# Kernel tuning notes

Measured on AMD Instinct MI355X. Metric: run time of the kernel, lower is better.

## Reference

```python
import jax, jax.numpy as jnp
import numpy as np

E = 1024      # emb_size == hidden_size
H = 8         # n_heads
BATCH = 8
NUM = 48      # table rows
KW = 48       # table columns (keys)
L = NUM * KW  # 2304


def _mha(q_in, kv_in, length, Wq, bq, Wk, bk, Wv, bv, Wo, bo, n_heads=H):
    # q_in: (B, T, E), kv_in: (B, S, E); returns (T, B, E) per the torch layout.
    B, T, Em = q_in.shape
    S = kv_in.shape[1]
    dh = Em // n_heads
    q = (q_in @ Wq + bq).reshape(B, T, n_heads, dh).transpose(0, 2, 1, 3)
    k = (kv_in @ Wk + bk).reshape(B, S, n_heads, dh).transpose(0, 2, 1, 3)
    v = (kv_in @ Wv + bv).reshape(B, S, n_heads, dh).transpose(0, 2, 1, 3)
    scores = jnp.einsum('bhtd,bhsd->bhts', q, k) / jnp.asarray(np.sqrt(dh), q.dtype)
    mask = jnp.arange(S) < length  # memory_lengths masking
    scores = jnp.where(mask[None, None, None, :], scores, jnp.finfo(scores.dtype).min)
    attn = jax.nn.softmax(scores, axis=-1)
    out = jnp.einsum('bhts,bhsd->bhtd', attn, v).transpose(0, 2, 1, 3).reshape(B, T, Em)
    out = out @ Wo + bo
    return out.transpose(1, 0, 2)  # (T, B, E)


def setup_inputs() -> dict:
    key = jax.random.key(0)
    ks = jax.random.split(key, 24)

    def W(k, shape, s=0.03):
        return jax.random.normal(k, shape, dtype=jnp.float32) * s

    inp = {
        'emb': jax.random.normal(ks[0], (L, BATCH, E), dtype=jnp.float32),
        # col attention params
        'Wq_c': W(ks[1], (E, E)), 'bq_c': jnp.zeros((E,), jnp.float32),
        'Wk_c': W(ks[2], (E, E)), 'bk_c': jnp.zeros((E,), jnp.float32),
        'Wv_c': W(ks[3], (E, E)), 'bv_c': jnp.zeros((E,), jnp.float32),
        'Wo_c': W(ks[4], (E, E)), 'bo_c': jnp.zeros((E,), jnp.float32),
        # row attention params
        'Wq_r': W(ks[5], (E, E)), 'bq_r': jnp.zeros((E,), jnp.float32),
        'Wk_r': W(ks[6], (E, E)), 'bk_r': jnp.zeros((E,), jnp.float32),
        'Wv_r': W(ks[7], (E, E)), 'bv_r': jnp.zeros((E,), jnp.float32),
        'Wo_r': W(ks[8], (E, E)), 'bo_r': jnp.zeros((E,), jnp.float32),
        # fusion layers
        'W_gen': W(ks[9], (2 * E, E)),
        'W_mlp1': W(ks[10], (2 * E, E)),
        'W_mlp2': W(ks[11], (E, 1)),
        # scalar forward args
        'start_id': 0, 'end_id': L - 1,
        'num': NUM, 'num_tensor': NUM,
        'kw_num': KW, 'kw_num_tensor': KW,
        'batch': BATCH,
    }
    return inp


def reference(emb, Wq_c, bq_c, Wk_c, bk_c, Wv_c, bv_c, Wo_c, bo_c,
              Wq_r, bq_r, Wk_r, bk_r, Wv_r, bv_r, Wo_r, bo_r,
              W_gen, W_mlp1, W_mlp2,
              start_id, end_id, num, num_tensor, kw_num, kw_num_tensor, batch):
    Em = emb.shape[-1]
    length = end_id - start_id + 1  # = num * kw_num
    # emb.narrow(0, start_id, length): (L, batch, E)
    rep = emb[start_id:start_id + length]
    # -> (kw_num, batch*num, E)
    home_ply_rep = rep.transpose(1, 0, 2).reshape(batch * num, kw_num, Em).transpose(1, 0, 2)

    # --- column-dim encoding: attention over the `num` (row) axis ---
    col_mb = jnp.swapaxes(home_ply_rep.reshape(kw_num, batch, num, Em), 0, 2)  # (num, batch, kw, E)
    col_mb = col_mb.reshape(num, batch * kw_num, Em)
    col_q = col_mb.transpose(1, 0, 2)  # (batch*kw, num, E)
    col_rep = _mha(col_q, col_q, num_tensor, Wq_c, bq_c, Wk_c, bk_c, Wv_c, bv_c, Wo_c, bo_c)
    # (num, batch*kw, E) -> (kw_num, batch*num, E)
    col_dim_rep = jnp.swapaxes(col_rep.reshape(num, batch, kw_num, Em), 0, 2).reshape(kw_num, batch * num, Em)

    # --- row-dim encoding: attention over the `kw_num` (column) axis ---
    row_q = col_dim_rep.transpose(1, 0, 2)  # (batch*num, kw, E)
    row_dim_rep = _mha(row_q, row_q, kw_num_tensor, Wq_r, bq_r, Wk_r, bk_r, Wv_r, bv_r, Wo_r, bo_r)  # (kw, b*n, E)

    # --- fusion: concat + Linear + tanh, MLP scores, softmax over {row, col} ---
    gen_rep = jnp.tanh(jnp.concatenate([row_dim_rep, col_dim_rep], axis=-1) @ W_gen)

    def mlp_score(x):
        return jnp.tanh(jnp.concatenate([x, gen_rep], axis=-1) @ W_mlp1) @ W_mlp2  # (kw, b*n, 1)

    row_score = mlp_score(row_dim_rep)
    col_score = mlp_score(col_dim_rep)
    w = jax.nn.softmax(jnp.concatenate([row_score, col_score], axis=-1), axis=-1)  # (kw, b*n, 2)
    home_ply_memory_bank = w[..., 0:1] * row_dim_rep + w[..., 1:2] * col_dim_rep
    # no_fusion=True -> residual add
    home_ply_memory_bank = home_ply_memory_bank + home_ply_rep

    row_for_ptr = row_dim_rep.reshape(kw_num, batch, num, Em)
    col_for_ptr = col_dim_rep.reshape(kw_num, batch, num, Em)

    # row_aggregation == 'mean'
    home_ply_row_rep = home_ply_memory_bank.mean(axis=0)  # (batch*num, E)
    home_ply_row_rep = home_ply_row_rep.reshape(batch, num, Em).transpose(1, 0, 2)  # (num, batch, E)
    return (home_ply_row_rep, home_ply_memory_bank, col_for_ptr, row_for_ptr)
```

## Files before the change

### kernel.cpp

```cpp
#include <hip/hip_runtime.h>
#include <hip/hip_bf16.h>
#include <stdint.h>

typedef unsigned short u16;
typedef unsigned int   u32;
typedef __attribute__((ext_vector_type(4))) float f32x4;
typedef __attribute__((ext_vector_type(2))) float f32x2;
typedef __attribute__((ext_vector_type(8))) short s16x8;

#define DEV __device__ __forceinline__

static constexpr int EDIM  = 1024;
static constexpr int MROWS = 8 * 48 * 48;

DEV float b2f(u16 x) { u32 u = ((u32)x) << 16; float f; __builtin_memcpy(&f, &u, 4); return f; }
DEV u16 f2b(float f) {
    u32 u; __builtin_memcpy(&u, &f, 4);
    u32 r = (u + 0x7FFFu + ((u >> 16) & 1u)) >> 16;
    return (u16)r;
}

#define GLDS16(gsrc, ldst) __builtin_amdgcn_global_load_lds( \
    (const __attribute__((address_space(1))) u32*)(gsrc),    \
    (__attribute__((address_space(3))) u32*)(ldst), 16, 0, 0)

#define BAR()   __builtin_amdgcn_s_barrier()
#define LGKM0() asm volatile("s_waitcnt lgkmcnt(0)" ::: "memory")

enum { F_WRC = 1, F_PERM = 2, F_TANH = 4, F_SCORE = 8, F_OMAP1 = 16, F_OMAP2 = 32 };

struct GJob {
    const u16* A1; const u16* A2; const u16* Bt; const float* bias;
    u16* C; float* outF; const float* w2; float* score;
    int lda, lda2, ldc, KTOT, M, flags, tileEnd, pad;
};
struct GSet { int njobs, total; GJob j[2]; };

struct WJob { const float* src; u16* dst; int srcN, dstLd, kOff, nT, tileEnd, pad; };
struct WSet { int n, total; WJob j[11]; };

__global__ void wconvJ_kernel(WSet ws) {
    int bid = blockIdx.x;
    int ji = 0;
    while (bid >= ws.j[ji].tileEnd) ++ji;
    int base = ji ? ws.j[ji - 1].tileEnd : 0;
    WJob J = ws.j[ji];
    int lt = bid - base;
    int n0 = (lt % J.nT) * 64, k0 = (lt / J.nT) * 64;
    __shared__ u16 tile[64][65];
    int tx = threadIdx.x & 63, ty = threadIdx.x >> 6;
#pragma unroll
    for (int i = 0; i < 16; ++i) {
        int r = ty * 16 + i;
        tile[r][tx] = f2b(J.src[(size_t)(k0 + r) * J.srcN + n0 + tx]);
    }
    __syncthreads();
#pragma unroll
    for (int i = 0; i < 16; ++i) {
        int r = ty * 16 + i;
        J.dst[(size_t)(n0 + r) * J.dstLd + J.kOff + k0 + tx] = tile[tx][r];
    }
}

__global__ void misc_kernel(const float* WoCsrc, const float* WoRsrc,
                            u16* WoCnt, u16* WoRnt,
                            const float* bq_c, const float* bk_c, const float* bv_c, float* bqkvC,
                            const float* bq_r, const float* bk_r, const float* bv_r,
                            const float* bo_c, const u16* WqkvRT, float* bqkvR_eff,
                            const float* bo_r, const u16* WgaT, float* bgen_lin,
                            float* scores) {
    int id = blockIdx.x * 256 + threadIdx.x;
    const int C1 = 1024 * 1024 / 2;
    if (id < C1) {
        f32x2 v = *(const f32x2*)&WoCsrc[(size_t)id * 2];
        *(u32*)&WoCnt[(size_t)id * 2] = (u32)f2b(v.x) | ((u32)f2b(v.y) << 16);
        return;
    }
    id -= C1;
    if (id < C1) {
        f32x2 v = *(const f32x2*)&WoRsrc[(size_t)id * 2];
        *(u32*)&WoRnt[(size_t)id * 2] = (u32)f2b(v.x) | ((u32)f2b(v.y) << 16);
        return;
    }
    id -= C1;
    if (id < 3072) { bqkvC[id] = (id < 1024) ? bq_c[id] : (id < 2048) ? bk_c[id - 1024] : bv_c[id - 2048]; return; }
    id -= 3072;
    if (id < 2 * MROWS) { scores[id] = 0.f; return; }
    id -= 2 * MROWS;
    if (id < 3072) {
        float s = (id < 1024) ? bq_r[id] : (id < 2048) ? bk_r[id - 1024] : bv_r[id - 2048];
        float d = 0.f;
        const u16* row = &WqkvRT[(size_t)id * 1024];
        for (int e = 0; e < 1024; e += 8) {
            s16x8 v = *(const s16x8*)&row[e];
#pragma unroll
            for (int u = 0; u < 8; ++u) d += bo_c[e + u] * b2f((u16)v[u]);
        }
        bqkvR_eff[id] = s + d;
        return;
    }
    id -= 3072;
    if (id < 1024) {
        float d = 0.f;
        const u16* row = &WgaT[(size_t)id * 1024];
        for (int e = 0; e < 1024; e += 8) {
            s16x8 v = *(const s16x8*)&row[e];
#pragma unroll
            for (int u = 0; u < 8; ++u) d += bo_r[e + u] * b2f((u16)v[u]);
        }
        bgen_lin[id] = d;
    }
}

__global__ void gather_kernel(const float* __restrict__ emb, u16* __restrict__ Xc) {
    int gid = blockIdx.x * 256 + threadIdx.x;
    int r = gid >> 9, c2 = gid & 511;
    int b = r / 2304, k = (r / 48) % 48, n = r % 48;
    int src = (n * 48 + k) * 8 + b;
    f32x2 v = *(const f32x2*)&emb[(size_t)src * EDIM + c2 * 2];
    *(u32*)&Xc[(size_t)r * EDIM + c2 * 2] = (u32)f2b(v.x) | ((u32)f2b(v.y) << 16);
}

DEV s16x8 ldsrd(const u16* lds, int r, int kk, int qq) {
    int gl = kk * 4 + qq;
    return *(const s16x8*)&lds[r * 64 + ((gl ^ (r & 7)) << 3)];
}
DEV void stageA_p(u16* lds, const u16* Ag, int lda, int m0, int ka, int h, int wv, int lane) {
#pragma unroll
    for (int i = 0; i < 2; ++i) {
        int blk = wv * 2 + i;
        int row0 = (h + 2 * (blk >> 3)) * 64 + (blk & 7) * 8;
        int rr = row0 + (lane >> 3);
        int gl = (lane & 7) ^ (rr & 7);
        GLDS16(Ag + (size_t)(m0 + rr) * lda + ka + gl * 8, lds + row0 * 64);
    }
}
DEV void stageB_p(u16* lds, const u16* Bg, int ldb, int n0, int kb, int h, int wv, int lane) {
#pragma unroll
    for (int i = 0; i < 2; ++i) {
        int blk = wv * 2 + i;
        int row0 = (blk >> 2) * 64 + h * 32 + (blk & 3) * 8;
        int rr = row0 + (lane >> 3);
        int gl = (lane & 7) ^ (rr & 7);
        GLDS16(Bg + (size_t)(n0 + rr) * ldb + kb + gl * 8, lds + row0 * 64);
    }
}

__global__ __launch_bounds__(512, 2) void gemmP_kernel(GSet js) {
    __shared__ u16 lA[2][256 * 64];
    __shared__ u16 lB[2][256 * 64];
    int tid = threadIdx.x, lane = tid & 63, wv = tid >> 6;
    int wm = wv >> 2, wn = wv & 3;
    int fr = lane & 15, qq = lane >> 4;
    int G = gridDim.x;
    int tIdx = blockIdx.x;
    if (tIdx >= js.total) return;

    int cm0, cn0, cNT, cji, nm0, nn0, nNT, nji;
    bool hasN;
    auto resolve = [&](int ti, int& m0, int& n0, int& NT, int& ji) {
        int j = (js.njobs > 1 && ti >= js.j[0].tileEnd) ? 1 : 0;
        int lt = ti - (j ? js.j[0].tileEnd : 0);
        int mtl = js.j[j].M >> 8;
        m0 = (lt % mtl) * 256; n0 = (lt / mtl) * 256;
        NT = js.j[j].KTOT >> 6; ji = j;
    };
    resolve(tIdx, cm0, cn0, cNT, cji);
    int tN = tIdx + G;
    hasN = tN < js.total;
    if (hasN) resolve(tN, nm0, nn0, nNT, nji);

    auto stA = [&](int dstbuf, int td, int h) -> bool {
        const GJob* J; int m0, kk;
        if (td < cNT) { J = &js.j[cji]; m0 = cm0; kk = td * 64; }
        else { int u = td - cNT; if (!hasN || u >= nNT) return false;
               J = &js.j[nji]; m0 = nm0; kk = u * 64; }
        const u16* Ag = J->A1; int lda = J->lda;
        if (J->A2 && kk >= 1024) { Ag = J->A2; lda = J->lda2; kk -= 1024; }
        stageA_p(&lA[dstbuf][0], Ag, lda, m0, kk, h, wv, lane);
        return true;
    };
    auto stB = [&](int dstbuf, int td, int h) -> bool {
        const GJob* J; int n0, kk;
        if (td < cNT) { J = &js.j[cji]; n0 = cn0; kk = td * 64; }
        else { int u = td - cNT; if (!hasN || u >= nNT) return false;
               J = &js.j[nji]; n0 = nn0; kk = u * 64; }
        stageB_p(&lB[dstbuf][0], J->Bt, J->KTOT, n0, kk, h, wv, lane);
        return true;
    };

    f32x4 acc[8][4];
#pragma unroll
    for (int i = 0; i < 8; ++i)
#pragma unroll
        for (int jj = 0; jj < 4; ++jj) acc[i][jj] = (f32x4)0.f;

    stA(0, 0, 0); stA(0, 0, 1); stB(0, 0, 0); stB(0, 0, 1);
    stA(1, 1, 0); stB(1, 1, 0); stB(1, 1, 1);
    asm volatile("s_waitcnt vmcnt(6)" ::: "memory");
    BAR();

    s16x8 A8[8], B0[4], B1[4];
    int buf = 0, t = 0;
    for (;;) {
        const u16* lAb = &lA[buf][0];
        const u16* lBb = &lB[buf][0];

#pragma unroll
        for (int m = 0; m < 4; ++m)
#pragma unroll
            for (int kk = 0; kk < 2; ++kk)
                A8[m * 2 + kk] = ldsrd(lAb, wm * 128 + m * 16 + fr, kk, qq);
#pragma unroll
        for (int n = 0; n < 2; ++n)
#pragma unroll
            for (int kk = 0; kk < 2; ++kk)
                B0[n * 2 + kk] = ldsrd(lBb, wn * 64 + n * 16 + fr, kk, qq);
        bool h1ex = stA(buf ^ 1, t + 1, 1);
        LGKM0();
        __builtin_amdgcn_s_setprio(1);
#pragma unroll
        for (int m = 0; m < 4; ++m)
#pragma unroll
            for (int n = 0; n < 2; ++n)
#pragma unroll
                for (int kk = 0; kk < 2; ++kk)
                    acc[m][n] = __builtin_amdgcn_mfma_f32_16x16x32_bf16(
                        A8[m * 2 + kk], B0[n * 2 + kk], acc[m][n], 0, 0, 0);
        __builtin_amdgcn_s_setprio(0);
        BAR();

#pragma unroll
        for (int n = 0; n < 2; ++n)
#pragma unroll
            for (int kk = 0; kk < 2; ++kk)
                B1[n * 2 + kk] = ldsrd(lBb, wn * 64 + 32 + n * 16 + fr, kk, qq);
        bool h2ex = stA(buf, t + 2, 0);
        LGKM0();
        __builtin_amdgcn_s_setprio(1);
#pragma unroll
        for (int m = 0; m < 4; ++m)
#pragma unroll
            for (int n = 0; n < 2; ++n)
#pragma unroll
                for (int kk = 0; kk < 2; ++kk)
                    acc[m][n + 2] = __builtin_amdgcn_mfma_f32_16x16x32_bf16(
                        A8[m * 2 + kk], B1[n * 2 + kk], acc[m][n + 2], 0, 0, 0);
        __builtin_amdgcn_s_setprio(0);
        BAR();

#pragma unroll
        for (int m = 0; m < 4; ++m)
#pragma unroll
            for (int kk = 0; kk < 2; ++kk)
                A8[m * 2 + kk] = ldsrd(lAb, wm * 128 + 64 + m * 16 + fr, kk, qq);
        stB(buf, t + 2, 0);
        LGKM0();
        __builtin_amdgcn_s_setprio(1);
#pragma unroll
        for (int m = 0; m < 4; ++m)
#pragma unroll
            for (int n = 0; n < 2; ++n)
#pragma unroll
                for (int kk = 0; kk < 2; ++kk)
                    acc[m + 4][n] = __builtin_amdgcn_mfma_f32_16x16x32_bf16(
                        A8[m * 2 + kk], B0[n * 2 + kk], acc[m + 4][n], 0, 0, 0);
        __builtin_amdgcn_s_setprio(0);
        BAR();

        stB(buf, t + 2, 1);
        __builtin_amdgcn_s_setprio(1);
#pragma unroll
        for (int m = 0; m < 4; ++m)
#pragma unroll
            for (int n = 0; n < 2; ++n)
#pragma unroll
                for (int kk = 0; kk < 2; ++kk)
                    acc[m + 4][n + 2] = __builtin_amdgcn_mfma_f32_16x16x32_bf16(
                        A8[m * 2 + kk], B1[n * 2 + kk], acc[m + 4][n + 2], 0, 0, 0);
        __builtin_amdgcn_s_setprio(0);
        if (h2ex)      asm volatile("s_waitcnt vmcnt(6)" ::: "memory");
        else if (h1ex) asm volatile("s_waitcnt vmcnt(0)" ::: "memory");
        BAR();

        buf ^= 1; ++t;
        if (t == cNT) {
            GJob J = js.j[cji];
            int crow4 = qq * 4;
#pragma unroll
            for (int mf = 0; mf < 8; ++mf) {
#pragma unroll
                for (int jj = 0; jj < 4; ++jj) {
                    int row = cm0 + wm * 128 + mf * 16 + crow4 + jj;
                    int orow = row, o32 = 0;
                    if (J.flags & (F_PERM | F_OMAP1)) {
                        int b = row / 2304, k = (row / 48) % 48, n = row % 48;
                        if (J.flags & F_PERM)  orow = (b * 48 + n) * 48 + k;
                        if (J.flags & F_OMAP1) o32 = k * 384 + b * 48 + n;
                    }
                    if (J.flags & F_OMAP2) {
                        int b = row / 2304, n = (row / 48) % 48, k = row % 48;
                        o32 = k * 384 + b * 48 + n;
                    }
                    float sc = 0.f;
#pragma unroll
                    for (int nf = 0; nf < 4; ++nf) {
                        int col = cn0 + wn * 64 + nf * 16 + fr;
                        float v = acc[mf][nf][jj];
                        if (J.bias) v += J.bias[col];
                        if (J.flags & F_TANH) v = tanhf(v);
                        if (J.flags & F_WRC) J.C[(size_t)orow * J.ldc + col] = f2b(v);
                        if (J.flags & (F_OMAP1 | F_OMAP2)) J.outF[(size_t)o32 * EDIM + col] = v;
                        if (J.flags & F_SCORE) sc += v * J.w2[col];
                    }
                    if (J.flags & F_SCORE) {
                        sc += __shfl_xor(sc, 1);
                        sc += __shfl_xor(sc, 2);
                        sc += __shfl_xor(sc, 4);
                        sc += __shfl_xor(sc, 8);
                        if (fr == 0) atomicAdd(&J.score[row], sc);
                    }
                }
            }
            if (!hasN) break;
#pragma unroll
            for (int i = 0; i < 8; ++i)
#pragma unroll
                for (int jj = 0; jj < 4; ++jj) acc[i][jj] = (f32x4)0.f;
            cm0 = nm0; cn0 = nn0; cNT = nNT; cji = nji;
            tN += G;
            hasN = tN < js.total;
            if (hasN) resolve(tN, nm0, nn0, nNT, nji);
            t = 0;
        }
    }
}

__global__ __launch_bounds__(64) void attn_kernel(u16* __restrict__ QKV) {
    __shared__ u16 lVt[128 * 72];
    __shared__ u16 lP[48 * 72];
    const int LDQ = 3072;
    int bb = blockIdx.x >> 3, h = blockIdx.x & 7;
    int lane = threadIdx.x;
    u16* Qp = QKV + (size_t)bb * 48 * LDQ + h * 128;
    const u16* Kp = Qp + 1024;
    const u16* Vp = Qp + 2048;

#pragma unroll
    for (int i = 0; i < 48; ++i) {
        u32 vv = *(const u32*)&Vp[(size_t)i * LDQ + lane * 2];
        lVt[(lane * 2) * 72 + i]     = (u16)(vv & 0xffffu);
        lVt[(lane * 2 + 1) * 72 + i] = (u16)(vv >> 16);
    }
    for (int i = lane; i < 128 * 16; i += 64) { int d = i >> 4, c = 48 + (i & 15); lVt[d * 72 + c] = 0; }
    for (int i = lane; i < 48 * 16; i += 64)  { int t = i >> 4, c = 48 + (i & 15); lP[t * 72 + c] = 0; }
    __syncthreads();

    int fr = lane & 15, fk = (lane >> 4) * 8, crow4 = (lane >> 4) * 4;
    f32x4 sc[3][3];
#pragma unroll
    for (int mf = 0; mf < 3; ++mf)
#pragma unroll
        for (int nf = 0; nf < 3; ++nf) sc[mf][nf] = (f32x4)0.f;

#pragma unroll
    for (int kk = 0; kk < 4; ++kk) {
        s16x8 aq[3], bk[3];
#pragma unroll
        for (int mf = 0; mf < 3; ++mf) aq[mf] = *(const s16x8*)&Qp[(size_t)(mf * 16 + fr) * LDQ + kk * 32 + fk];
#pragma unroll
        for (int nf = 0; nf < 3; ++nf) bk[nf] = *(const s16x8*)&Kp[(size_t)(nf * 16 + fr) * LDQ + kk * 32 + fk];
#pragma unroll
        for (int mf = 0; mf < 3; ++mf)
#pragma unroll
            for (int nf = 0; nf < 3; ++nf)
                sc[mf][nf] = __builtin_amdgcn_mfma_f32_16x16x32_bf16(aq[mf], bk[nf], sc[mf][nf], 0, 0, 0);
    }

    const float scale = 0.08838834764831845f;
#pragma unroll
    for (int mf = 0; mf < 3; ++mf) {
#pragma unroll
        for (int j = 0; j < 4; ++j) {
            float v0 = sc[mf][0][j] * scale;
            float v1 = sc[mf][1][j] * scale;
            float v2 = sc[mf][2][j] * scale;
            float mx = fmaxf(v0, fmaxf(v1, v2));
            mx = fmaxf(mx, __shfl_xor(mx, 1));
            mx = fmaxf(mx, __shfl_xor(mx, 2));
            mx = fmaxf(mx, __shfl_xor(mx, 4));
            mx = fmaxf(mx, __shfl_xor(mx, 8));
            float e0 = __expf(v0 - mx), e1 = __expf(v1 - mx), e2 = __expf(v2 - mx);
            float s = e0 + e1 + e2;
            s += __shfl_xor(s, 1);
            s += __shfl_xor(s, 2);
            s += __shfl_xor(s, 4);
            s += __shfl_xor(s, 8);
            float inv = 1.f / s;
            int t = mf * 16 + crow4 + j;
            lP[t * 72 + 0  + fr] = f2b(e0 * inv);
            lP[t * 72 + 16 + fr] = f2b(e1 * inv);
            lP[t * 72 + 32 + fr] = f2b(e2 * inv);
        }
    }
    __syncthreads();

    f32x4 o[3][8];
#pragma unroll
    for (int mf = 0; mf < 3; ++mf)
#pragma unroll
        for (int nf = 0; nf < 8; ++nf) o[mf][nf] = (f32x4)0.f;

#pragma unroll
    for (int kk = 0; kk < 2; ++kk) {
        s16x8 ap[3];
#pragma unroll
        for (int mf = 0; mf < 3; ++mf) ap[mf] = *(const s16x8*)&lP[(mf * 16 + fr) * 72 + kk * 32 + fk];
#pragma unroll
        for (int nf = 0; nf < 8; ++nf) {
            s16x8 bv = *(const s16x8*)&lVt[(nf * 16 + fr) * 72 + kk * 32 + fk];
#pragma unroll
            for (int mf = 0; mf < 3; ++mf)
                o[mf][nf] = __builtin_amdgcn_mfma_f32_16x16x32_bf16(ap[mf], bv, o[mf][nf], 0, 0, 0);
        }
    }
#pragma unroll
    for (int mf = 0; mf < 3; ++mf)
#pragma unroll
        for (int nf = 0; nf < 8; ++nf)
#pragma unroll
            for (int j = 0; j < 4; ++j) {
                int t = mf * 16 + crow4 + j, d = nf * 16 + fr;
                Qp[(size_t)t * LDQ + d] = f2b(o[mf][nf][j]);
            }
}

__global__ void combine_mean_kernel(const u16* __restrict__ RDR, const u16* __restrict__ CDR,
                                    const float* __restrict__ srow, const float* __restrict__ scol,
                                    const float* __restrict__ emb, float* __restrict__ out) {
    int b = blockIdx.x / 48, n = blockIdx.x % 48;
    __shared__ float w0s[48], w1s[48];
    int tx = threadIdx.x;
    if (tx < 48) {
        int r2 = (b * 48 + n) * 48 + tx;
        float rs = srow[r2], cs = scol[r2];
        float m = fmaxf(rs, cs);
        float e0 = __expf(rs - m), e1 = __expf(cs - m);
        float inv = 1.f / (e0 + e1);
        w0s[tx] = e0 * inv; w1s[tx] = e1 * inv;
    }
    __syncthreads();
    float* out_mb = out + 393216;
    for (int e = tx; e < EDIM; e += 256) {
        float s = 0.f;
        for (int k = 0; k < 48; ++k) {
            size_t rb = (size_t)((b * 48 + n) * 48 + k) * EDIM;
            float rv = b2f(RDR[rb + e]);
            float cv = b2f(CDR[rb + e]);
            float hv = emb[((size_t)(n * 48 + k) * 8 + b) * EDIM + e];
            float v = w0s[k] * rv + w1s[k] * cv + hv;
            out_mb[(size_t)(k * 384 + b * 48 + n) * EDIM + e] = v;
            s += v;
        }
        out[(size_t)(n * 8 + b) * EDIM + e] = s * (1.f / 48.f);
    }
}

extern "C" void kernel_launch(void* const* d_in, const int* in_sizes, int n_in,
                              void* d_out, int out_size, void* d_ws, size_t ws_size,
                              hipStream_t stream) {
    const float* emb    = (const float*)d_in[0];
    const float* Wq_c   = (const float*)d_in[1];
    const float* bq_c   = (const float*)d_in[2];
    const float* Wk_c   = (const float*)d_in[3];
    const float* bk_c   = (const float*)d_in[4];
    const float* Wv_c   = (const float*)d_in[5];
    const float* bv_c   = (const float*)d_in[6];
    const float* Wo_c   = (const float*)d_in[7];
    const float* bo_c   = (const float*)d_in[8];
    const float* Wq_r   = (const float*)d_in[9];
    const float* bq_r   = (const float*)d_in[10];
    const float* Wk_r   = (const float*)d_in[11];
    const float* bk_r   = (const float*)d_in[12];
    const float* Wv_r   = (const float*)d_in[13];
    const float* bv_r   = (const float*)d_in[14];
    const float* Wo_r   = (const float*)d_in[15];
    const float* bo_r   = (const float*)d_in[16];
    const float* W_gen  = (const float*)d_in[17];
    const float* W_mlp1 = (const float*)d_in[18];
    const float* W_mlp2 = (const float*)d_in[19];
    (void)in_sizes; (void)n_in; (void)out_size; (void)ws_size;

    char* ws = (char*)d_ws;
    size_t off = 0;
    auto alloc = [&](size_t bytes) { char* p = ws + off; off += (bytes + 255) & ~(size_t)255; return p; };
    u16*   WqkvCT = (u16*)alloc((size_t)3072 * 1024 * 2);
    u16*   WqkvRT = (u16*)alloc((size_t)3072 * 1024 * 2);
    u16*   WoCT   = (u16*)alloc((size_t)1024 * 1024 * 2);
    u16*   WoRT   = (u16*)alloc((size_t)1024 * 1024 * 2);
    u16*   WoCnt  = (u16*)alloc((size_t)1024 * 1024 * 2);
    u16*   WoRnt  = (u16*)alloc((size_t)1024 * 1024 * 2);
    u16*   WgaT   = (u16*)alloc((size_t)1024 * 1024 * 2);
    u16*   BtGf   = (u16*)alloc((size_t)1024 * 2048 * 2);
    u16*   W1T    = (u16*)alloc((size_t)1024 * 2048 * 2);
    u16*   BtQKVr = (u16*)alloc((size_t)3072 * 1024 * 2);
    float* bqkvC  = (float*)alloc(3072 * 4);
    float* bqkvRe = (float*)alloc(3072 * 4);
    float* bgen   = (float*)alloc(1024 * 4);
    u16*   XA     = (u16*)alloc((size_t)MROWS * 1024 * 2);
    u16*   QKV    = (u16*)alloc((size_t)MROWS * 3072 * 2);
    u16*   QKV2   = (u16*)alloc((size_t)MROWS * 3072 * 2);
    u16*   CDR    = (u16*)alloc((size_t)MROWS * 1024 * 2);
    u16*   RDR    = (u16*)alloc((size_t)MROWS * 1024 * 2);
    float* score_row = (float*)alloc((size_t)MROWS * 4);
    float* score_col = (float*)alloc((size_t)MROWS * 4);

    float* out = (float*)d_out;
    float* out_col = out + 393216 + 18874368;
    float* out_row = out + 393216 + 2 * 18874368;

    dim3 tb(256), tb512(512);

    WSet wset = {};
    int te = 0;
    auto addW = [&](const float* src, u16* dst, int srcN, int dstLd, int kOff, int nT, int kT) {
        int i = wset.n++;
        te += nT * kT;
        WJob w = {src, dst, srcN, dstLd, kOff, nT, te, 0};
        wset.j[i] = w;
    };
    addW(Wq_c, WqkvCT,                   1024, 1024, 0, 16, 16);
    addW(Wk_c, WqkvCT + 1024 * 1024,     1024, 1024, 0, 16, 16);
    addW(Wv_c, WqkvCT + 2 * 1024 * 1024, 1024, 1024, 0, 16, 16);
    addW(Wo_c, WoCT,                     1024, 1024, 0, 16, 16);
    addW(Wq_r, WqkvRT,                   1024, 1024, 0, 16, 16);
    addW(Wk_r, WqkvRT + 1024 * 1024,     1024, 1024, 0, 16, 16);
    addW(Wv_r, WqkvRT + 2 * 1024 * 1024, 1024, 1024, 0, 16, 16);
    addW(Wo_r, WoRT,                     1024, 1024, 0, 16, 16);
    addW(W_gen,               WgaT,      1024, 1024, 0, 16, 16);
    addW(W_gen + 1024 * 1024, BtGf,      1024, 2048, 1024, 16, 16);
    addW(W_mlp1,              W1T,       1024, 2048, 0, 16, 32);
    wset.total = te;
    wconvJ_kernel<<<te, tb, 0, stream>>>(wset);

    int miscItems = 1024 * 1024 + 3072 + 2 * MROWS + 3072 + 1024;
    misc_kernel<<<(miscItems + 255) / 256, tb, 0, stream>>>(
        Wo_c, Wo_r, WoCnt, WoRnt,
        bq_c, bk_c, bv_c, bqkvC,
        bq_r, bk_r, bv_r,
        bo_c, WqkvRT, bqkvRe,
        bo_r, WgaT, bgen,
        score_row);

    gather_kernel<<<MROWS * 512 / 256, tb, 0, stream>>>(emb, XA);

    auto mkJob = [](const u16* A1, const u16* A2, const u16* Bt, const float* bias,
                    u16* C, float* outF, const float* w2, float* score,
                    int lda, int lda2, int ldc, int KTOT, int M, int flags) {
        GJob j = {A1, A2, Bt, bias, C, outF, w2, score, lda, lda2, ldc, KTOT, M, flags, 0, 0};
        return j;
    };
    auto run1 = [&](GJob a, int nA) {
        GSet gs = {};
        a.tileEnd = (a.M >> 8) * nA;
        gs.njobs = 1; gs.total = a.tileEnd; gs.j[0] = a;
        gemmP_kernel<<<256, tb512, 0, stream>>>(gs);
    };
    auto run2 = [&](GJob a, int nA, GJob b, int nB) {
        GSet gs = {};
        a.tileEnd = (a.M >> 8) * nA;
        b.tileEnd = a.tileEnd + (b.M >> 8) * nB;
        gs.njobs = 2; gs.total = b.tileEnd; gs.j[0] = a; gs.j[1] = b;
        gemmP_kernel<<<256, tb512, 0, stream>>>(gs);
    };

    run2(mkJob(WqkvRT, nullptr, WoCnt, nullptr, BtQKVr, nullptr, nullptr, nullptr,
               1024, 0, 1024, 1024, 3072, F_WRC), 4,
         mkJob(WgaT, nullptr, WoRnt, nullptr, BtGf, nullptr, nullptr, nullptr,
               1024, 0, 2048, 1024, 1024, F_WRC), 4);

    run1(mkJob(XA, nullptr, WqkvCT, bqkvC, QKV, nullptr, nullptr, nullptr,
               1024, 0, 3072, 1024, MROWS, F_WRC), 12);
    attn_kernel<<<384 * 8, 64, 0, stream>>>(QKV);
    run2(mkJob(QKV, nullptr, WoCT, bo_c, CDR, out_col, nullptr, nullptr,
               3072, 0, 1024, 1024, MROWS, F_WRC | F_PERM | F_OMAP1), 4,
         mkJob(QKV, nullptr, BtQKVr, bqkvRe, QKV2, nullptr, nullptr, nullptr,
               3072, 0, 3072, 1024, MROWS, F_WRC | F_PERM), 12);
    attn_kernel<<<384 * 8, 64, 0, stream>>>(QKV2);
    run2(mkJob(QKV2, nullptr, WoRT, bo_r, RDR, out_row, nullptr, nullptr,
               3072, 0, 1024, 1024, MROWS, F_WRC | F_OMAP2), 4,
         mkJob(QKV2, CDR, BtGf, bgen, XA, nullptr, nullptr, nullptr,
               3072, 1024, 1024, 2048, MROWS, F_WRC | F_TANH), 4);
    run2(mkJob(RDR, XA, W1T, nullptr, nullptr, nullptr, W_mlp2, score_row,
               1024, 1024, 1024, 2048, MROWS, F_SCORE | F_TANH), 4,
         mkJob(CDR, XA, W1T, nullptr, nullptr, nullptr, W_mlp2, score_col,
               1024, 1024, 1024, 2048, MROWS, F_SCORE | F_TANH), 4);

    combine_mean_kernel<<<384, tb, 0, stream>>>(RDR, CDR, score_row, score_col, emb, out);
}
```

Measured before the change: 1.319 ms.

## Replace persistent 256-tile GEMM with simple 128-tile kernel and factor shared MLP term

Replaces the persistent, deeply pipelined 256x256 GEMM (512 threads, staggered half-tile staging) with a simpler 128x128 tile kernel (256 threads, K-step 32, double buffer), launched with one block per tile. It also merges the weight-prep GEMMs into the first projection launch. The MLP layer is split so that gen_rep @ W1b is computed once into an fp32 buffer and added in the epilogue of both score GEMMs, which removes a duplicated half of that work. The simpler kernel may lose the prior software pipelining efficiency, and the fp32 intermediate adds memory traffic.

```diff
diff --git a/kernel.cpp b/kernel.cpp
--- a/kernel.cpp
+++ b/kernel.cpp
@@ -24,20 +24,18 @@
     (const __attribute__((address_space(1))) u32*)(gsrc),    \
     (__attribute__((address_space(3))) u32*)(ldst), 16, 0, 0)
 
-#define BAR()   __builtin_amdgcn_s_barrier()
-#define LGKM0() asm volatile("s_waitcnt lgkmcnt(0)" ::: "memory")
-
-enum { F_WRC = 1, F_PERM = 2, F_TANH = 4, F_SCORE = 8, F_OMAP1 = 16, F_OMAP2 = 32 };
+enum { F_WRC = 1, F_PERM = 2, F_TANH = 4, F_SCORE = 8, F_OMAP1 = 16, F_OMAP2 = 32,
+       F_OUTFLIN = 64, F_HGEN = 128 };
 
 struct GJob {
     const u16* A1; const u16* A2; const u16* Bt; const float* bias;
     u16* C; float* outF; const float* w2; float* score;
     int lda, lda2, ldc, KTOT, M, flags, tileEnd, pad;
 };
-struct GSet { int njobs, total; GJob j[2]; };
+struct GSet3 { int njobs, pad; GJob j[3]; };
 
 struct WJob { const float* src; u16* dst; int srcN, dstLd, kOff, nT, tileEnd, pad; };
-struct WSet { int n, total; WJob j[11]; };
+struct WSet { int n, total; WJob j[12]; };
 
 __global__ void wconvJ_kernel(WSet ws) {
     int bid = blockIdx.x;
@@ -121,217 +119,105 @@
     *(u32*)&Xc[(size_t)r * EDIM + c2 * 2] = (u32)f2b(v.x) | ((u32)f2b(v.y) << 16);
 }
 
-DEV s16x8 ldsrd(const u16* lds, int r, int kk, int qq) {
-    int gl = kk * 4 + qq;
-    return *(const s16x8*)&lds[r * 64 + ((gl ^ (r & 7)) << 3)];
-}
-DEV void stageA_p(u16* lds, const u16* Ag, int lda, int m0, int ka, int h, int wv, int lane) {
-#pragma unroll
-    for (int i = 0; i < 2; ++i) {
-        int blk = wv * 2 + i;
-        int row0 = (h + 2 * (blk >> 3)) * 64 + (blk & 7) * 8;
-        int rr = row0 + (lane >> 3);
-        int gl = (lane & 7) ^ (rr & 7);
-        GLDS16(Ag + (size_t)(m0 + rr) * lda + ka + gl * 8, lds + row0 * 64);
-    }
-}
-DEV void stageB_p(u16* lds, const u16* Bg, int ldb, int n0, int kb, int h, int wv, int lane) {
-#pragma unroll
-    for (int i = 0; i < 2; ++i) {
-        int blk = wv * 2 + i;
-        int row0 = (blk >> 2) * 64 + h * 32 + (blk & 3) * 8;
-        int rr = row0 + (lane >> 3);
-        int gl = (lane & 7) ^ (rr & 7);
-        GLDS16(Bg + (size_t)(n0 + rr) * ldb + kb + gl * 8, lds + row0 * 64);
-    }
-}
-
-__global__ __launch_bounds__(512, 2) void gemmP_kernel(GSet js) {
-    __shared__ u16 lA[2][256 * 64];
-    __shared__ u16 lB[2][256 * 64];
+__global__ __launch_bounds__(256, 4) void gemmJ_kernel(GSet3 js) {
+    __shared__ u16 lA[2][128 * 32];
+    __shared__ u16 lB[2][128 * 32];
+    int bid = blockIdx.x;
+    int ji = 0, base = 0;
+    if (js.njobs > 1 && bid >= js.j[0].tileEnd) { ji = 1; base = js.j[0].tileEnd; }
+    if (js.njobs > 2 && bid >= js.j[1].tileEnd) { ji = 2; base = js.j[1].tileEnd; }
+    GJob J;
+    if (ji == 0) J = js.j[0]; else if (ji == 1) J = js.j[1]; else J = js.j[2];
+
+    int lt = bid - base;
+    int mtl = J.M >> 7;
+    int mt = lt % mtl, nt = lt / mtl;
+    int m0 = mt * 128, n0 = nt * 128;
     int tid = threadIdx.x, lane = tid & 63, wv = tid >> 6;
-    int wm = wv >> 2, wn = wv & 3;
+    int wm = wv >> 1, wn = wv & 1;
     int fr = lane & 15, qq = lane >> 4;
-    int G = gridDim.x;
-    int tIdx = blockIdx.x;
-    if (tIdx >= js.total) return;
-
-    int cm0, cn0, cNT, cji, nm0, nn0, nNT, nji;
-    bool hasN;
-    auto resolve = [&](int ti, int& m0, int& n0, int& NT, int& ji) {
-        int j = (js.njobs > 1 && ti >= js.j[0].tileEnd) ? 1 : 0;
-        int lt = ti - (j ? js.j[0].tileEnd : 0);
-        int mtl = js.j[j].M >> 8;
-        m0 = (lt % mtl) * 256; n0 = (lt / mtl) * 256;
-        NT = js.j[j].KTOT >> 6; ji = j;
+    int NT = J.KTOT >> 5;
+
+    f32x4 acc[4][4];
+#pragma unroll
+    for (int i = 0; i < 4; ++i)
+#pragma unroll
+        for (int jj = 0; jj < 4; ++jj) acc[i][jj] = (f32x4)0.f;
+
+    auto STAGE = [&](int bsel, int kt) {
+        int k0 = kt * 32;
+        const u16* As = J.A1; int lda = J.lda; int ka = k0;
+        if (J.A2 && k0 >= 1024) { As = J.A2; lda = J.lda2; ka = k0 - 1024; }
+#pragma unroll
+        for (int i = 0; i < 2; ++i) {
+            int c = wv * 2 + i;
+            int r = c * 16 + (lane >> 2);
+            int qg = ((lane & 3) - (r >> 1)) & 3;
+            GLDS16(As + (size_t)(m0 + r) * lda + ka + qg * 8, &lA[bsel][c * 512]);
+            GLDS16(J.Bt + (size_t)(n0 + r) * J.KTOT + k0 + qg * 8, &lB[bsel][c * 512]);
+        }
     };
-    resolve(tIdx, cm0, cn0, cNT, cji);
-    int tN = tIdx + G;
-    hasN = tN < js.total;
-    if (hasN) resolve(tN, nm0, nn0, nNT, nji);
-
-    auto stA = [&](int dstbuf, int td, int h) -> bool {
-        const GJob* J; int m0, kk;
-        if (td < cNT) { J = &js.j[cji]; m0 = cm0; kk = td * 64; }
-        else { int u = td - cNT; if (!hasN || u >= nNT) return false;
-               J = &js.j[nji]; m0 = nm0; kk = u * 64; }
-        const u16* Ag = J->A1; int lda = J->lda;
-        if (J->A2 && kk >= 1024) { Ag = J->A2; lda = J->lda2; kk -= 1024; }
-        stageA_p(&lA[dstbuf][0], Ag, lda, m0, kk, h, wv, lane);
-        return true;
-    };
-    auto stB = [&](int dstbuf, int td, int h) -> bool {
-        const GJob* J; int n0, kk;
-        if (td < cNT) { J = &js.j[cji]; n0 = cn0; kk = td * 64; }
-        else { int u = td - cNT; if (!hasN || u >= nNT) return false;
-               J = &js.j[nji]; n0 = nn0; kk = u * 64; }
-        stageB_p(&lB[dstbuf][0], J->Bt, J->KTOT, n0, kk, h, wv, lane);
-        return true;
-    };
-
-    f32x4 acc[8][4];
-#pragma unroll
-    for (int i = 0; i < 8; ++i)
-#pragma unroll
-        for (int jj = 0; jj < 4; ++jj) acc[i][jj] = (f32x4)0.f;
-
-    stA(0, 0, 0); stA(0, 0, 1); stB(0, 0, 0); stB(0, 0, 1);
-    stA(1, 1, 0); stB(1, 1, 0); stB(1, 1, 1);
-    asm volatile("s_waitcnt vmcnt(6)" ::: "memory");
-    BAR();
-
-    s16x8 A8[8], B0[4], B1[4];
-    int buf = 0, t = 0;
-    for (;;) {
-        const u16* lAb = &lA[buf][0];
-        const u16* lBb = &lB[buf][0];
-
-#pragma unroll
-        for (int m = 0; m < 4; ++m)
-#pragma unroll
-            for (int kk = 0; kk < 2; ++kk)
-                A8[m * 2 + kk] = ldsrd(lAb, wm * 128 + m * 16 + fr, kk, qq);
-#pragma unroll
-        for (int n = 0; n < 2; ++n)
-#pragma unroll
-            for (int kk = 0; kk < 2; ++kk)
-                B0[n * 2 + kk] = ldsrd(lBb, wn * 64 + n * 16 + fr, kk, qq);
-        bool h1ex = stA(buf ^ 1, t + 1, 1);
-        LGKM0();
-        __builtin_amdgcn_s_setprio(1);
-#pragma unroll
-        for (int m = 0; m < 4; ++m)
-#pragma unroll
-            for (int n = 0; n < 2; ++n)
-#pragma unroll
-                for (int kk = 0; kk < 2; ++kk)
-                    acc[m][n] = __builtin_amdgcn_mfma_f32_16x16x32_bf16(
-                        A8[m * 2 + kk], B0[n * 2 + kk], acc[m][n], 0, 0, 0);
-        __builtin_amdgcn_s_setprio(0);
-        BAR();
-
-#pragma unroll
-        for (int n = 0; n < 2; ++n)
-#pragma unroll
-            for (int kk = 0; kk < 2; ++kk)
-                B1[n * 2 + kk] = ldsrd(lBb, wn * 64 + 32 + n * 16 + fr, kk, qq);
-        bool h2ex = stA(buf, t + 2, 0);
-        LGKM0();
-        __builtin_amdgcn_s_setprio(1);
-#pragma unroll
-        for (int m = 0; m < 4; ++m)
-#pragma unroll
-            for (int n = 0; n < 2; ++n)
-#pragma unroll
-                for (int kk = 0; kk < 2; ++kk)
-                    acc[m][n + 2] = __builtin_amdgcn_mfma_f32_16x16x32_bf16(
-                        A8[m * 2 + kk], B1[n * 2 + kk], acc[m][n + 2], 0, 0, 0);
-        __builtin_amdgcn_s_setprio(0);
-        BAR();
-
-#pragma unroll
-        for (int m = 0; m < 4; ++m)
-#pragma unroll
-            for (int kk = 0; kk < 2; ++kk)
-                A8[m * 2 + kk] = ldsrd(lAb, wm * 128 + 64 + m * 16 + fr, kk, qq);
-        stB(buf, t + 2, 0);
-        LGKM0();
-        __builtin_amdgcn_s_setprio(1);
-#pragma unroll
-        for (int m = 0; m < 4; ++m)
-#pragma unroll
-            for (int n = 0; n < 2; ++n)
-#pragma unroll
-                for (int kk = 0; kk < 2; ++kk)
-                    acc[m + 4][n] = __builtin_amdgcn_mfma_f32_16x16x32_bf16(
-                        A8[m * 2 + kk], B0[n * 2 + kk], acc[m + 4][n], 0, 0, 0);
-        __builtin_amdgcn_s_setprio(0);
-        BAR();
-
-        stB(buf, t + 2, 1);
-        __builtin_amdgcn_s_setprio(1);
-#pragma unroll
-        for (int m = 0; m < 4; ++m)
-#pragma unroll
-            for (int n = 0; n < 2; ++n)
-#pragma unroll
-                for (int kk = 0; kk < 2; ++kk)
-                    acc[m + 4][n + 2] = __builtin_amdgcn_mfma_f32_16x16x32_bf16(
-                        A8[m * 2 + kk], B1[n * 2 + kk], acc[m + 4][n + 2], 0, 0, 0);
-        __builtin_amdgcn_s_setprio(0);
-        if (h2ex)      asm volatile("s_waitcnt vmcnt(6)" ::: "memory");
-        else if (h1ex) asm volatile("s_waitcnt vmcnt(0)" ::: "memory");
-        BAR();
-
-        buf ^= 1; ++t;
-        if (t == cNT) {
-            GJob J = js.j[cji];
-            int crow4 = qq * 4;
-#pragma unroll
-            for (int mf = 0; mf < 8; ++mf) {
-#pragma unroll
-                for (int jj = 0; jj < 4; ++jj) {
-                    int row = cm0 + wm * 128 + mf * 16 + crow4 + jj;
-                    int orow = row, o32 = 0;
-                    if (J.flags & (F_PERM | F_OMAP1)) {
-                        int b = row / 2304, k = (row / 48) % 48, n = row % 48;
-                        if (J.flags & F_PERM)  orow = (b * 48 + n) * 48 + k;
-                        if (J.flags & F_OMAP1) o32 = k * 384 + b * 48 + n;
-                    }
-                    if (J.flags & F_OMAP2) {
-                        int b = row / 2304, n = (row / 48) % 48, k = row % 48;
-                        o32 = k * 384 + b * 48 + n;
-                    }
-                    float sc = 0.f;
-#pragma unroll
-                    for (int nf = 0; nf < 4; ++nf) {
-                        int col = cn0 + wn * 64 + nf * 16 + fr;
-                        float v = acc[mf][nf][jj];
-                        if (J.bias) v += J.bias[col];
-                        if (J.flags & F_TANH) v = tanhf(v);
-                        if (J.flags & F_WRC) J.C[(size_t)orow * J.ldc + col] = f2b(v);
-                        if (J.flags & (F_OMAP1 | F_OMAP2)) J.outF[(size_t)o32 * EDIM + col] = v;
-                        if (J.flags & F_SCORE) sc += v * J.w2[col];
-                    }
-                    if (J.flags & F_SCORE) {
-                        sc += __shfl_xor(sc, 1);
-                        sc += __shfl_xor(sc, 2);
-                        sc += __shfl_xor(sc, 4);
-                        sc += __shfl_xor(sc, 8);
-                        if (fr == 0) atomicAdd(&J.score[row], sc);
-                    }
-                }
+
+    STAGE(0, 0);
+    for (int kt = 0; kt < NT; ++kt) {
+        __syncthreads();
+        if (kt + 1 < NT) STAGE((kt + 1) & 1, kt + 1);
+        const u16* la = &lA[kt & 1][0];
+        const u16* lb = &lB[kt & 1][0];
+        s16x8 af[4], bf[4];
+#pragma unroll
+        for (int mf = 0; mf < 4; ++mf) {
+            int rr = wm * 64 + mf * 16 + fr;
+            af[mf] = *(const s16x8*)&la[rr * 32 + (((qq + (rr >> 1)) & 3) * 8)];
+        }
+#pragma unroll
+        for (int nf = 0; nf < 4; ++nf) {
+            int rn = wn * 64 + nf * 16 + fr;
+            bf[nf] = *(const s16x8*)&lb[rn * 32 + (((qq + (rn >> 1)) & 3) * 8)];
+        }
+#pragma unroll
+        for (int mf = 0; mf < 4; ++mf)
+#pragma unroll
+            for (int nf = 0; nf < 4; ++nf)
+                acc[mf][nf] = __builtin_amdgcn_mfma_f32_16x16x32_bf16(af[mf], bf[nf], acc[mf][nf], 0, 0, 0);
+    }
+
+    int crow4 = qq * 4;
+#pragma unroll
+    for (int mf = 0; mf < 4; ++mf) {
+#pragma unroll
+        for (int jj = 0; jj < 4; ++jj) {
+            int row = m0 + wm * 64 + mf * 16 + crow4 + jj;
+            int orow = row, o32 = 0;
+            if (J.flags & (F_PERM | F_OMAP1)) {
+                int b = row / 2304, k = (row / 48) % 48, n = row % 48;
+                if (J.flags & F_PERM)  orow = (b * 48 + n) * 48 + k;
+                if (J.flags & F_OMAP1) o32 = k * 384 + b * 48 + n;
             }
-            if (!hasN) break;
-#pragma unroll
-            for (int i = 0; i < 8; ++i)
-#pragma unroll
-                for (int jj = 0; jj < 4; ++jj) acc[i][jj] = (f32x4)0.f;
-            cm0 = nm0; cn0 = nn0; cNT = nNT; cji = nji;
-            tN += G;
-            hasN = tN < js.total;
-            if (hasN) resolve(tN, nm0, nn0, nNT, nji);
-            t = 0;
+            if (J.flags & F_OMAP2) {
+                int b = row / 2304, n = (row / 48) % 48, k = row % 48;
+                o32 = k * 384 + b * 48 + n;
+            }
+            float sc = 0.f;
+#pragma unroll
+            for (int nf = 0; nf < 4; ++nf) {
+                int col = n0 + wn * 64 + nf * 16 + fr;
+                float v = acc[mf][nf][jj];
+                if (J.bias) v += J.bias[col];
+                if (J.flags & F_HGEN) v += J.outF[(size_t)row * EDIM + col];
+                if (J.flags & F_TANH) v = tanhf(v);
+                if (J.flags & F_WRC) J.C[(size_t)orow * J.ldc + col] = f2b(v);
+                if (J.flags & (F_OMAP1 | F_OMAP2)) J.outF[(size_t)o32 * EDIM + col] = v;
+                if (J.flags & F_OUTFLIN) J.outF[(size_t)row * EDIM + col] = v;
+                if (J.flags & F_SCORE) sc += v * J.w2[col];
+            }
+            if (J.flags & F_SCORE) {
+                sc += __shfl_xor(sc, 1);
+                sc += __shfl_xor(sc, 2);
+                sc += __shfl_xor(sc, 4);
+                sc += __shfl_xor(sc, 8);
+                if (fr == 0) atomicAdd(&J.score[row], sc);
+            }
         }
     }
 }
@@ -502,7 +388,8 @@
     u16*   WoRnt  = (u16*)alloc((size_t)1024 * 1024 * 2);
     u16*   WgaT   = (u16*)alloc((size_t)1024 * 1024 * 2);
     u16*   BtGf   = (u16*)alloc((size_t)1024 * 2048 * 2);
-    u16*   W1T    = (u16*)alloc((size_t)1024 * 2048 * 2);
+    u16*   W1aT   = (u16*)alloc((size_t)1024 * 1024 * 2);
+    u16*   W1bT   = (u16*)alloc((size_t)1024 * 1024 * 2);
     u16*   BtQKVr = (u16*)alloc((size_t)3072 * 1024 * 2);
     float* bqkvC  = (float*)alloc(3072 * 4);
     float* bqkvRe = (float*)alloc(3072 * 4);
@@ -514,12 +401,13 @@
     u16*   RDR    = (u16*)alloc((size_t)MROWS * 1024 * 2);
     float* score_row = (float*)alloc((size_t)MROWS * 4);
     float* score_col = (float*)alloc((size_t)MROWS * 4);
+    float* Hgen = (float*)QKV;
 
     float* out = (float*)d_out;
     float* out_col = out + 393216 + 18874368;
     float* out_row = out + 393216 + 2 * 18874368;
 
-    dim3 tb(256), tb512(512);
+    dim3 tb(256);
 
     WSet wset = {};
     int te = 0;
@@ -539,7 +427,8 @@
     addW(Wo_r, WoRT,                     1024, 1024, 0, 16, 16);
     addW(W_gen,               WgaT,      1024, 1024, 0, 16, 16);
     addW(W_gen + 1024 * 1024, BtGf,      1024, 2048, 1024, 16, 16);
-    addW(W_mlp1,              W1T,       1024, 2048, 0, 16, 32);
+    addW(W_mlp1,               W1aT,     1024, 1024, 0, 16, 16);
+    addW(W_mlp1 + 1024 * 1024, W1bT,     1024, 1024, 0, 16, 16);
     wset.total = te;
     wconvJ_kernel<<<te, tb, 0, stream>>>(wset);
 
@@ -560,41 +449,55 @@
         GJob j = {A1, A2, Bt, bias, C, outF, w2, score, lda, lda2, ldc, KTOT, M, flags, 0, 0};
         return j;
     };
-    auto run1 = [&](GJob a, int nA) {
-        GSet gs = {};
-        a.tileEnd = (a.M >> 8) * nA;
-        gs.njobs = 1; gs.total = a.tileEnd; gs.j[0] = a;
-        gemmP_kernel<<<256, tb512, 0, stream>>>(gs);
+    auto runJ = [&](GJob a, int nA, const GJob* b, int nB, const GJob* c, int nC) {
+        GSet3 gs = {};
+        a.tileEnd = (a.M >> 7) * nA;
+        gs.j[0] = a;
+        int tot = a.tileEnd, nj = 1;
+        if (b) {
+            GJob jb = *b;
+            jb.tileEnd = tot + (jb.M >> 7) * nB;
+            tot = jb.tileEnd; gs.j[1] = jb; nj = 2;
+        }
+        if (c) {
+            GJob jc = *c;
+            jc.tileEnd = tot + (jc.M >> 7) * nC;
+            tot = jc.tileEnd; gs.j[2] = jc; nj = 3;
+        }
+        gs.njobs = nj;
+        gemmJ_kernel<<<tot, tb, 0, stream>>>(gs);
     };
-    auto run2 = [&](GJob a, int nA, GJob b, int nB) {
-        GSet gs = {};
-        a.tileEnd = (a.M >> 8) * nA;
-        b.tileEnd = a.tileEnd + (b.M >> 8) * nB;
-        gs.njobs = 2; gs.total = b.tileEnd; gs.j[0] = a; gs.j[1] = b;
-        gemmP_kernel<<<256, tb512, 0, stream>>>(gs);
-    };
-
-    run2(mkJob(WqkvRT, nullptr, WoCnt, nullptr, BtQKVr, nullptr, nullptr, nullptr,
-               1024, 0, 1024, 1024, 3072, F_WRC), 4,
-         mkJob(WgaT, nullptr, WoRnt, nullptr, BtGf, nullptr, nullptr, nullptr,
-               1024, 0, 2048, 1024, 1024, F_WRC), 4);
-
-    run1(mkJob(XA, nullptr, WqkvCT, bqkvC, QKV, nullptr, nullptr, nullptr,
-               1024, 0, 3072, 1024, MROWS, F_WRC), 12);
+
+    {
+        GJob b = mkJob(WqkvRT, nullptr, WoCnt, nullptr, BtQKVr, nullptr, nullptr, nullptr,
+                       1024, 0, 1024, 1024, 3072, F_WRC);
+        GJob c = mkJob(WgaT, nullptr, WoRnt, nullptr, BtGf, nullptr, nullptr, nullptr,
+                       1024, 0, 2048, 1024, 1024, F_WRC);
+        runJ(mkJob(XA, nullptr, WqkvCT, bqkvC, QKV, nullptr, nullptr, nullptr,
+                   1024, 0, 3072, 1024, MROWS, F_WRC), 24, &b, 8, &c, 8);
+    }
     attn_kernel<<<384 * 8, 64, 0, stream>>>(QKV);
-    run2(mkJob(QKV, nullptr, WoCT, bo_c, CDR, out_col, nullptr, nullptr,
-               3072, 0, 1024, 1024, MROWS, F_WRC | F_PERM | F_OMAP1), 4,
-         mkJob(QKV, nullptr, BtQKVr, bqkvRe, QKV2, nullptr, nullptr, nullptr,
-               3072, 0, 3072, 1024, MROWS, F_WRC | F_PERM), 12);
+    {
+        GJob b = mkJob(QKV, nullptr, BtQKVr, bqkvRe, QKV2, nullptr, nullptr, nullptr,
+                       3072, 0, 3072, 1024, MROWS, F_WRC | F_PERM);
+        runJ(mkJob(QKV, nullptr, WoCT, bo_c, CDR, out_col, nullptr, nullptr,
+                   3072, 0, 1024, 1024, MROWS, F_WRC | F_PERM | F_OMAP1), 8, &b, 24, nullptr, 0);
+    }
     attn_kernel<<<384 * 8, 64, 0, stream>>>(QKV2);
-    run2(mkJob(QKV2, nullptr, WoRT, bo_r, RDR, out_row, nullptr, nullptr,
-               3072, 0, 1024, 1024, MROWS, F_WRC | F_OMAP2), 4,
-         mkJob(QKV2, CDR, BtGf, bgen, XA, nullptr, nullptr, nullptr,
-               3072, 1024, 1024, 2048, MROWS, F_WRC | F_TANH), 4);
-    run2(mkJob(RDR, XA, W1T, nullptr, nullptr, nullptr, W_mlp2, score_row,
-               1024, 1024, 1024, 2048, MROWS, F_SCORE | F_TANH), 4,
-         mkJob(CDR, XA, W1T, nullptr, nullptr, nullptr, W_mlp2, score_col,
-               1024, 1024, 1024, 2048, MROWS, F_SCORE | F_TANH), 4);
+    {
+        GJob b = mkJob(QKV2, CDR, BtGf, bgen, XA, nullptr, nullptr, nullptr,
+                       3072, 1024, 1024, 2048, MROWS, F_WRC | F_TANH);
+        runJ(mkJob(QKV2, nullptr, WoRT, bo_r, RDR, out_row, nullptr, nullptr,
+                   3072, 0, 1024, 1024, MROWS, F_WRC | F_OMAP2), 8, &b, 8, nullptr, 0);
+    }
+    runJ(mkJob(XA, nullptr, W1bT, nullptr, nullptr, Hgen, nullptr, nullptr,
+               1024, 0, 1024, 1024, MROWS, F_OUTFLIN), 8, nullptr, 0, nullptr, 0);
+    {
+        GJob b = mkJob(CDR, nullptr, W1aT, nullptr, nullptr, Hgen, W_mlp2, score_col,
+                       1024, 0, 1024, 1024, MROWS, F_SCORE | F_TANH | F_HGEN);
+        runJ(mkJob(RDR, nullptr, W1aT, nullptr, nullptr, Hgen, W_mlp2, score_row,
+                   1024, 0, 1024, 1024, MROWS, F_SCORE | F_TANH | F_HGEN), 8, &b, 8, nullptr, 0);
+    }
 
     combine_mean_kernel<<<384, tb, 0, stream>>>(RDR, CDR, score_row, score_col, emb, out);
 }
```

Measured after the change: 1.110 ms. 1.19x faster.
